# Performance work log

Hardware: AMD Instinct MI355X
Metric: run time of the kernel (lower is better)

Reference implementation:

```python
import jax, jax.numpy as jnp
import numpy as np

N, M, D = 8192, 8192, 64

def setup_inputs() -> dict:
    key = jax.random.key(0)
    kx, ky = jax.random.split(key)
    x = jax.random.normal(kx, (N, D), dtype=jnp.float32)
    y = jax.random.normal(ky, (M, D), dtype=jnp.float32)
    return {"x": x, "y": y}

def reference(x, y):
    T = 1.0
    # Dmat = 2 - euclidean cdist(x, y), computed via the Gram trick.
    sq = (jnp.sum(x * x, axis=1)[:, None]
          + jnp.sum(y * y, axis=1)[None, :]
          - 2.0 * (x @ y.T))
    Dmat = 2.0 - jnp.sqrt(jnp.maximum(sq, 0.0))          # [N, M]
    logprob_rows = jax.nn.log_softmax(Dmat * T, axis=1)   # [N, M]
    logprob_cols = jax.nn.log_softmax(Dmat.T * T, axis=1) # [M, N]
    choice_rows = jnp.argmax(logprob_rows, axis=1)        # [N]
    choice_cols = jnp.argmax(logprob_cols, axis=1)        # [M]
    seq = jnp.arange(M, dtype=choice_cols.dtype)
    mutual = choice_rows[choice_cols] == seq              # [M] bool
    lp_rows = jnp.take_along_axis(logprob_rows, choice_rows[:, None], axis=1)[:, 0]  # [N]
    lp_cols = jnp.take_along_axis(logprob_cols, choice_cols[:, None], axis=1)[:, 0]  # [M]
    # Padded (jit-friendly) form of the boolean compaction: entries where
    # mutual is False are zeroed; mutual mask identifies valid matches.
    log_probs = jnp.where(mutual, lp_rows[choice_cols] + lp_cols, 0.0)  # [M]
    dmatches = jnp.stack([choice_cols, seq], axis=1)      # [M, 2]
    return (log_probs, dmatches, mutual)
```

## Files before the change

### kernel.cpp

```cpp
#include <hip/hip_runtime.h>
#include <stdint.h>

#define NROWS 8192
#define MCOLS 8192
#define DDIM  64

typedef _Float16 half8   __attribute__((ext_vector_type(8)));
typedef float    floatx4 __attribute__((ext_vector_type(4)));

__device__ __forceinline__ unsigned f2key(float f) {
  unsigned u = __float_as_uint(f);
  return (u & 0x80000000u) ? ~u : (u | 0x80000000u);
}
__device__ __forceinline__ float key2f(unsigned k) {
  unsigned u = (k & 0x80000000u) ? (k & 0x7fffffffu) : ~k;
  return __uint_as_float(u);
}

__global__ void convert_kernel(const float* __restrict__ x, const float* __restrict__ y,
                               _Float16* __restrict__ xh, _Float16* __restrict__ xl,
                               _Float16* __restrict__ yh, _Float16* __restrict__ yl,
                               float* __restrict__ xn, float* __restrict__ yn,
                               unsigned long long* __restrict__ rk,
                               unsigned long long* __restrict__ ck,
                               float* __restrict__ rs, float* __restrict__ cs) {
  __shared__ float lnorm[32];
  const int gid = blockIdx.x * 256 + threadIdx.x;
  if (gid < 8192) { rk[gid] = 0ull; rs[gid] = 0.0f; ck[gid] = 0ull; cs[gid] = 0.0f; }
  if (threadIdx.x < 32) lnorm[threadIdx.x] = 0.0f;
  __syncthreads();

  const float* src; _Float16 *dh, *dl; float* nout; int t, rowbase;
  if (gid < 65536) { src = x; dh = xh; dl = xl; nout = xn; t = gid;
                     rowbase = blockIdx.x * 32; }
  else             { src = y; dh = yh; dl = yl; nout = yn; t = gid - 65536;
                     rowbase = (blockIdx.x - 256) * 32; }

  const int lane = t & 63;
  const int c    = (t >> 6) & 1;
  const int p    = t >> 7;
  const int row  = p * 16 + (lane & 15);
  const int k0   = c * 32 + ((lane >> 4) << 3);
  const float* s = src + (size_t)row * DDIM + k0;

  _Float16 hbuf[8], lbuf[8];
  float s8 = 0.0f;
  #pragma unroll
  for (int j = 0; j < 8; ++j) {
    float f = s[j];
    _Float16 h = (_Float16)f;
    hbuf[j] = h;
    lbuf[j] = (_Float16)((f - (float)h) * 2048.0f);
    s8 = fmaf(f, f, s8);
  }
  size_t o = (size_t)t * 8;
  *(half8*)(dh + o) = *(half8*)hbuf;
  *(half8*)(dl + o) = *(half8*)lbuf;

  atomicAdd(&lnorm[((p & 1) << 4) | (t & 15)], s8);
  __syncthreads();
  if (threadIdx.x < 32) nout[rowbase + threadIdx.x] = lnorm[threadIdx.x];
}

__global__ __launch_bounds__(256, 4) void mfma_tile_kernel(
    const _Float16* __restrict__ xh, const _Float16* __restrict__ xl,
    const _Float16* __restrict__ yh, const _Float16* __restrict__ yl,
    const float* __restrict__ xn, const float* __restrict__ yn,
    unsigned long long* __restrict__ row_key, float* __restrict__ row_sum,
    unsigned long long* __restrict__ col_key, float* __restrict__ col_sum)
{
  __shared__ unsigned long long lkey[256];
  __shared__ float              lsum[256];

  const int wave = threadIdx.x >> 6;
  const int lane = threadIdx.x & 63;
  const int l15  = lane & 15;
  const int g    = lane >> 4;
  const int ap0  = blockIdx.y * 8 + wave * 2;
  const int ro   = ap0 * 16 + g * 4;
  const int colbase = blockIdx.x * 256;

  lkey[threadIdx.x] = 0ull;
  lsum[threadIdx.x] = 0.0f;
  __syncthreads();

  const half8* xh8 = (const half8*)xh;
  const half8* xl8 = (const half8*)xl;
  const half8* yh8 = (const half8*)yh;
  const half8* yl8 = (const half8*)yl;
  const size_t a0 = (size_t)ap0 * 128 + lane;
  half8 Ah[2][2], Al[2][2];
  #pragma unroll
  for (int p = 0; p < 2; ++p) {
    Ah[p][0] = xh8[a0 + p * 128];      Ah[p][1] = xh8[a0 + p * 128 + 64];
    Al[p][0] = xl8[a0 + p * 128];      Al[p][1] = xl8[a0 + p * 128 + 64];
  }

  float xne[8], rsum[8], rmax[8]; int ridx[8];
  #pragma unroll
  for (int s = 0; s < 8; ++s) {
    xne[s]  = xn[ro + ((s >> 2) << 4) + (s & 3)];
    rsum[s] = 0.0f; rmax[s] = -3.4e38f; ridx[s] = 0;
  }

  for (int jt = 0; jt < 16; ++jt) {
    const size_t b0 = (size_t)(blockIdx.x * 16 + jt) * 128 + lane;
    const half8 bh0 = yh8[b0], bh1 = yh8[b0 + 64];
    const half8 bl0 = yl8[b0], bl1 = yl8[b0 + 64];
    const int col = colbase + jt * 16 + l15;
    const float ync = yn[col];

    float dv[8], ev[8];
    #pragma unroll
    for (int p = 0; p < 2; ++p) {
      floatx4 c1 = {}, c2 = {};
      c1 = __builtin_amdgcn_mfma_f32_16x16x32_f16(Ah[p][0], bh0, c1, 0, 0, 0);
      c1 = __builtin_amdgcn_mfma_f32_16x16x32_f16(Ah[p][1], bh1, c1, 0, 0, 0);
      c2 = __builtin_amdgcn_mfma_f32_16x16x32_f16(Al[p][0], bh0, c2, 0, 0, 0);
      c2 = __builtin_amdgcn_mfma_f32_16x16x32_f16(Al[p][1], bh1, c2, 0, 0, 0);
      c2 = __builtin_amdgcn_mfma_f32_16x16x32_f16(Ah[p][0], bl0, c2, 0, 0, 0);
      c2 = __builtin_amdgcn_mfma_f32_16x16x32_f16(Ah[p][1], bl1, c2, 0, 0, 0);
      #pragma unroll
      for (int r = 0; r < 4; ++r) {
        const int s = p * 4 + r;
        float dot = fmaf(c2[r], (1.0f / 2048.0f), c1[r]);
        float sq  = fmaxf(fmaf(-2.0f, dot, xne[s] + ync), 0.0f);
        float d   = 2.0f - __builtin_amdgcn_sqrtf(sq);
        float e   = __expf(d);
        rsum[s] += e;
        if (d > rmax[s]) ridx[s] = col;
        rmax[s] = fmaxf(rmax[s], d);
        dv[s] = d; ev[s] = e;
      }
    }

    float m01 = fmaxf(dv[0], dv[1]); int i01 = dv[1] > dv[0] ? 1 : 0;
    float m23 = fmaxf(dv[2], dv[3]); int i23 = dv[3] > dv[2] ? 3 : 2;
    float m45 = fmaxf(dv[4], dv[5]); int i45 = dv[5] > dv[4] ? 5 : 4;
    float m67 = fmaxf(dv[6], dv[7]); int i67 = dv[7] > dv[6] ? 7 : 6;
    float mA  = fmaxf(m01, m23);     int iA  = m23 > m01 ? i23 : i01;
    float mB  = fmaxf(m45, m67);     int iB  = m67 > m45 ? i67 : i45;
    float mC  = fmaxf(mA, mB);       int iC  = mB  > mA  ? iB  : iA;
    int crow  = ro + ((iC >> 2) << 4) + (iC & 3);
    float csum = ((ev[0] + ev[1]) + (ev[2] + ev[3])) + ((ev[4] + ev[5]) + (ev[6] + ev[7]));
    unsigned long long ckey =
        ((unsigned long long)f2key(mC) << 32) | (unsigned long long)(unsigned)(~(unsigned)crow);
    atomicMax(&lkey[jt * 16 + l15], ckey);
    atomicAdd(&lsum[jt * 16 + l15], csum);
  }

  unsigned long long rkk[8];
  #pragma unroll
  for (int s = 0; s < 8; ++s)
    rkk[s] = ((unsigned long long)f2key(rmax[s]) << 32) |
             (unsigned long long)(unsigned)(~(unsigned)ridx[s]);
  #pragma unroll
  for (int off = 1; off < 16; off <<= 1) {
    #pragma unroll
    for (int s = 0; s < 8; ++s) {
      rsum[s] += __shfl_xor(rsum[s], off);
      unsigned long long o = __shfl_xor(rkk[s], off);
      if (o > rkk[s]) rkk[s] = o;
    }
  }
  if (l15 == 0) {
    #pragma unroll
    for (int s = 0; s < 8; ++s) {
      int row = ro + ((s >> 2) << 4) + (s & 3);
      atomicMax(row_key + row, rkk[s]);
      atomicAdd(row_sum + row, rsum[s]);
    }
  }

  __syncthreads();
  {
    int col = colbase + threadIdx.x;
    atomicMax(col_key + col, lkey[threadIdx.x]);
    atomicAdd(col_sum + col, lsum[threadIdx.x]);
  }
}

__global__ void finalize_kernel(const unsigned long long* __restrict__ row_key,
                                const float* __restrict__ row_sum,
                                const unsigned long long* __restrict__ col_key,
                                const float* __restrict__ col_sum,
                                float* __restrict__ out)
{
  int j = blockIdx.x * 256 + threadIdx.x;
  if (j >= MCOLS) return;
  unsigned long long ck = col_key[j];
  int   ci   = (int)(~(unsigned)ck);
  float cmax = key2f((unsigned)(ck >> 32));
  float lp_col = cmax - logf(col_sum[j]);

  unsigned long long rk = row_key[ci];
  int   rj   = (int)(~(unsigned)rk);
  float rmax = key2f((unsigned)(rk >> 32));
  float lp_row = rmax - logf(row_sum[ci]);

  int mut = (rj == j);
  out[j]                 = mut ? (lp_row + lp_col) : 0.0f;
  out[MCOLS + 2 * j + 0] = (float)ci;
  out[MCOLS + 2 * j + 1] = (float)j;
  out[3 * MCOLS + j]     = mut ? 1.0f : 0.0f;
}

extern "C" void kernel_launch(void* const* d_in, const int* in_sizes, int n_in,
                              void* d_out, int out_size, void* d_ws, size_t ws_size,
                              hipStream_t stream) {
  const float* x = (const float*)d_in[0];
  const float* y = (const float*)d_in[1];
  float* out = (float*)d_out;

  char* ws = (char*)d_ws;
  unsigned long long* row_key = (unsigned long long*)(ws);
  unsigned long long* col_key = (unsigned long long*)(ws + 65536);
  float* row_sum = (float*)(ws + 131072);
  float* col_sum = (float*)(ws + 163840);
  float* xn      = (float*)(ws + 196608);
  float* yn      = (float*)(ws + 229376);
  _Float16* xh = (_Float16*)(ws + 262144);
  _Float16* xl = (_Float16*)(ws + 262144 + 1048576);
  _Float16* yh = (_Float16*)(ws + 262144 + 2097152);
  _Float16* yl = (_Float16*)(ws + 262144 + 3145728);

  convert_kernel<<<512, 256, 0, stream>>>(x, y, xh, xl, yh, yl, xn, yn,
                                          row_key, col_key, row_sum, col_sum);
  dim3 grid(MCOLS / 256, NROWS / 128);
  mfma_tile_kernel<<<grid, 256, 0, stream>>>(xh, xl, yh, yl, xn, yn,
                                             row_key, row_sum, col_key, col_sum);
  finalize_kernel<<<32, 256, 0, stream>>>(row_key, row_sum, col_key, col_sum, out);
}
```

Baseline: 128.3 us.

## Fuse finalize into tile kernel via last-block counter, widen column tile, prefetch B

Doubles the columns each block covers, which halves the grid and the global column atomics per element. It also prefetches the next B fragment in registers and folds the column max and sum into the inner loop in place of a tree reduction. The separate finalize kernel is removed: a global done counter elects the last block to compute outputs. The risk is that this last block runs the 8192-element epilogue alone, serialised at the end, and the halved grid (1024 blocks) may reduce occupancy and latency hiding.

```diff
diff --git a/kernel.cpp b/kernel.cpp
--- a/kernel.cpp
+++ b/kernel.cpp
@@ -23,10 +23,12 @@
                                float* __restrict__ xn, float* __restrict__ yn,
                                unsigned long long* __restrict__ rk,
                                unsigned long long* __restrict__ ck,
-                               float* __restrict__ rs, float* __restrict__ cs) {
+                               float* __restrict__ rs, float* __restrict__ cs,
+                               unsigned* __restrict__ done) {
   __shared__ float lnorm[32];
   const int gid = blockIdx.x * 256 + threadIdx.x;
   if (gid < 8192) { rk[gid] = 0ull; rs[gid] = 0.0f; ck[gid] = 0ull; cs[gid] = 0.0f; }
+  if (gid == 0) *done = 0u;
   if (threadIdx.x < 32) lnorm[threadIdx.x] = 0.0f;
   __syncthreads();
 
@@ -67,10 +69,12 @@
     const _Float16* __restrict__ yh, const _Float16* __restrict__ yl,
     const float* __restrict__ xn, const float* __restrict__ yn,
     unsigned long long* __restrict__ row_key, float* __restrict__ row_sum,
-    unsigned long long* __restrict__ col_key, float* __restrict__ col_sum)
+    unsigned long long* __restrict__ col_key, float* __restrict__ col_sum,
+    unsigned* __restrict__ done, float* __restrict__ out)
 {
-  __shared__ unsigned long long lkey[256];
-  __shared__ float              lsum[256];
+  __shared__ unsigned long long lkey[512];
+  __shared__ float              lsum[512];
+  __shared__ unsigned           lastflag;
 
   const int wave = threadIdx.x >> 6;
   const int lane = threadIdx.x & 63;
@@ -78,10 +82,12 @@
   const int g    = lane >> 4;
   const int ap0  = blockIdx.y * 8 + wave * 2;
   const int ro   = ap0 * 16 + g * 4;
-  const int colbase = blockIdx.x * 256;
-
-  lkey[threadIdx.x] = 0ull;
-  lsum[threadIdx.x] = 0.0f;
+  const int colbase = blockIdx.x * 512;
+
+  lkey[threadIdx.x]       = 0ull;
+  lkey[threadIdx.x + 256] = 0ull;
+  lsum[threadIdx.x]       = 0.0f;
+  lsum[threadIdx.x + 256] = 0.0f;
   __syncthreads();
 
   const half8* xh8 = (const half8*)xh;
@@ -103,14 +109,21 @@
     rsum[s] = 0.0f; rmax[s] = -3.4e38f; ridx[s] = 0;
   }
 
-  for (int jt = 0; jt < 16; ++jt) {
-    const size_t b0 = (size_t)(blockIdx.x * 16 + jt) * 128 + lane;
-    const half8 bh0 = yh8[b0], bh1 = yh8[b0 + 64];
-    const half8 bl0 = yl8[b0], bl1 = yl8[b0 + 64];
+  const size_t bbase = (size_t)(blockIdx.x * 32) * 128 + lane;
+  half8 nbh0 = yh8[bbase], nbh1 = yh8[bbase + 64];
+  half8 nbl0 = yl8[bbase], nbl1 = yl8[bbase + 64];
+
+  for (int jt = 0; jt < 32; ++jt) {
+    const half8 bh0 = nbh0, bh1 = nbh1, bl0 = nbl0, bl1 = nbl1;
     const int col = colbase + jt * 16 + l15;
     const float ync = yn[col];
-
-    float dv[8], ev[8];
+    if (jt < 31) {
+      const size_t nb = bbase + (size_t)(jt + 1) * 128;
+      nbh0 = yh8[nb];  nbh1 = yh8[nb + 64];
+      nbl0 = yl8[nb];  nbl1 = yl8[nb + 64];
+    }
+
+    float csum = 0.0f, cmax = -3.4e38f; int cs8 = 0;
     #pragma unroll
     for (int p = 0; p < 2; ++p) {
       floatx4 c1 = {}, c2 = {};
@@ -127,24 +140,17 @@
         float sq  = fmaxf(fmaf(-2.0f, dot, xne[s] + ync), 0.0f);
         float d   = 2.0f - __builtin_amdgcn_sqrtf(sq);
         float e   = __expf(d);
-        rsum[s] += e;
+        rsum[s] += e;  csum += e;
         if (d > rmax[s]) ridx[s] = col;
         rmax[s] = fmaxf(rmax[s], d);
-        dv[s] = d; ev[s] = e;
+        if (d > cmax) cs8 = s;
+        cmax = fmaxf(cmax, d);
       }
     }
 
-    float m01 = fmaxf(dv[0], dv[1]); int i01 = dv[1] > dv[0] ? 1 : 0;
-    float m23 = fmaxf(dv[2], dv[3]); int i23 = dv[3] > dv[2] ? 3 : 2;
-    float m45 = fmaxf(dv[4], dv[5]); int i45 = dv[5] > dv[4] ? 5 : 4;
-    float m67 = fmaxf(dv[6], dv[7]); int i67 = dv[7] > dv[6] ? 7 : 6;
-    float mA  = fmaxf(m01, m23);     int iA  = m23 > m01 ? i23 : i01;
-    float mB  = fmaxf(m45, m67);     int iB  = m67 > m45 ? i67 : i45;
-    float mC  = fmaxf(mA, mB);       int iC  = mB  > mA  ? iB  : iA;
-    int crow  = ro + ((iC >> 2) << 4) + (iC & 3);
-    float csum = ((ev[0] + ev[1]) + (ev[2] + ev[3])) + ((ev[4] + ev[5]) + (ev[6] + ev[7]));
+    int crow = ro + ((cs8 >> 2) << 4) + (cs8 & 3);
     unsigned long long ckey =
-        ((unsigned long long)f2key(mC) << 32) | (unsigned long long)(unsigned)(~(unsigned)crow);
+        ((unsigned long long)f2key(cmax) << 32) | (unsigned long long)(unsigned)(~(unsigned)crow);
     atomicMax(&lkey[jt * 16 + l15], ckey);
     atomicAdd(&lsum[jt * 16 + l15], csum);
   }
@@ -173,36 +179,43 @@
   }
 
   __syncthreads();
-  {
-    int col = colbase + threadIdx.x;
-    atomicMax(col_key + col, lkey[threadIdx.x]);
-    atomicAdd(col_sum + col, lsum[threadIdx.x]);
-  }
-}
-
-__global__ void finalize_kernel(const unsigned long long* __restrict__ row_key,
-                                const float* __restrict__ row_sum,
-                                const unsigned long long* __restrict__ col_key,
-                                const float* __restrict__ col_sum,
-                                float* __restrict__ out)
-{
-  int j = blockIdx.x * 256 + threadIdx.x;
-  if (j >= MCOLS) return;
-  unsigned long long ck = col_key[j];
-  int   ci   = (int)(~(unsigned)ck);
-  float cmax = key2f((unsigned)(ck >> 32));
-  float lp_col = cmax - logf(col_sum[j]);
-
-  unsigned long long rk = row_key[ci];
-  int   rj   = (int)(~(unsigned)rk);
-  float rmax = key2f((unsigned)(rk >> 32));
-  float lp_row = rmax - logf(row_sum[ci]);
-
-  int mut = (rj == j);
-  out[j]                 = mut ? (lp_row + lp_col) : 0.0f;
-  out[MCOLS + 2 * j + 0] = (float)ci;
-  out[MCOLS + 2 * j + 1] = (float)j;
-  out[3 * MCOLS + j]     = mut ? 1.0f : 0.0f;
+  #pragma unroll
+  for (int q = 0; q < 2; ++q) {
+    int t = threadIdx.x + q * 256;
+    atomicMax(col_key + colbase + t, lkey[t]);
+    atomicAdd(col_sum + colbase + t, lsum[t]);
+  }
+
+  __threadfence();
+  if (threadIdx.x == 0)
+    lastflag = (atomicAdd(done, 1u) == (16u * 64u - 1u)) ? 1u : 0u;
+  __syncthreads();
+  if (lastflag) {
+    __threadfence();
+    for (int j = threadIdx.x; j < MCOLS; j += 256) {
+      unsigned long long ck =
+          __hip_atomic_load(col_key + j, __ATOMIC_RELAXED, __HIP_MEMORY_SCOPE_AGENT);
+      float csv =
+          __hip_atomic_load(col_sum + j, __ATOMIC_RELAXED, __HIP_MEMORY_SCOPE_AGENT);
+      int   ci   = (int)(~(unsigned)ck);
+      float cmax = key2f((unsigned)(ck >> 32));
+      float lp_col = cmax - logf(csv);
+
+      unsigned long long rk =
+          __hip_atomic_load(row_key + ci, __ATOMIC_RELAXED, __HIP_MEMORY_SCOPE_AGENT);
+      float rsv =
+          __hip_atomic_load(row_sum + ci, __ATOMIC_RELAXED, __HIP_MEMORY_SCOPE_AGENT);
+      int   rj   = (int)(~(unsigned)rk);
+      float rmx  = key2f((unsigned)(rk >> 32));
+      float lp_row = rmx - logf(rsv);
+
+      int mut = (rj == j);
+      out[j]                 = mut ? (lp_row + lp_col) : 0.0f;
+      out[MCOLS + 2 * j + 0] = (float)ci;
+      out[MCOLS + 2 * j + 1] = (float)j;
+      out[3 * MCOLS + j]     = mut ? 1.0f : 0.0f;
+    }
+  }
 }
 
 extern "C" void kernel_launch(void* const* d_in, const int* in_sizes, int n_in,
@@ -223,11 +236,12 @@
   _Float16* xl = (_Float16*)(ws + 262144 + 1048576);
   _Float16* yh = (_Float16*)(ws + 262144 + 2097152);
   _Float16* yl = (_Float16*)(ws + 262144 + 3145728);
+  unsigned* done = (unsigned*)(ws + 262144 + 4194304);
 
   convert_kernel<<<512, 256, 0, stream>>>(x, y, xh, xl, yh, yl, xn, yn,
-                                          row_key, col_key, row_sum, col_sum);
-  dim3 grid(MCOLS / 256, NROWS / 128);
+                                          row_key, col_key, row_sum, col_sum, done);
+  dim3 grid(MCOLS / 512, NROWS / 128);
   mfma_tile_kernel<<<grid, 256, 0, stream>>>(xh, xl, yh, yl, xn, yn,
-                                             row_key, row_sum, col_key, col_sum);
-  finalize_kernel<<<32, 256, 0, stream>>>(row_key, row_sum, col_key, col_sum, out);
-}
+                                             row_key, row_sum, col_key, col_sum,
+                                             done, out);
+}
```

Measured after the change: 189.2 us. 47.5% more time.

## Prefetch next B tile in MFMA loop, simplify convert kernel and column argmax

Applied to the files above, without the earlier changes.

The MFMA tile loop now loads the next column tile's fp16 hi/lo fragments one iteration ahead, so global load latency overlaps with the current tile's compute. The per-tile column max/argmax and sum are tracked incrementally instead of through a stored array and a tree reduction. The convert kernel is rewritten to one element per thread with a wave shuffle reduction for the row norms, replacing LDS atomics, and is launched with more blocks. Risks: prefetching raises register pressure under launch bounds of 4 blocks per CU, and the scalar 2-byte stores in convert are less coalesced than the previous 16-byte vector stores.

```diff
diff --git a/kernel.cpp b/kernel.cpp
--- a/kernel.cpp
+++ b/kernel.cpp
@@ -24,42 +24,26 @@
                                unsigned long long* __restrict__ rk,
                                unsigned long long* __restrict__ ck,
                                float* __restrict__ rs, float* __restrict__ cs) {
-  __shared__ float lnorm[32];
-  const int gid = blockIdx.x * 256 + threadIdx.x;
-  if (gid < 8192) { rk[gid] = 0ull; rs[gid] = 0.0f; ck[gid] = 0ull; cs[gid] = 0.0f; }
-  if (threadIdx.x < 32) lnorm[threadIdx.x] = 0.0f;
-  __syncthreads();
-
-  const float* src; _Float16 *dh, *dl; float* nout; int t, rowbase;
-  if (gid < 65536) { src = x; dh = xh; dl = xl; nout = xn; t = gid;
-                     rowbase = blockIdx.x * 32; }
-  else             { src = y; dh = yh; dl = yl; nout = yn; t = gid - 65536;
-                     rowbase = (blockIdx.x - 256) * 32; }
-
-  const int lane = t & 63;
-  const int c    = (t >> 6) & 1;
-  const int p    = t >> 7;
-  const int row  = p * 16 + (lane & 15);
-  const int k0   = c * 32 + ((lane >> 4) << 3);
-  const float* s = src + (size_t)row * DDIM + k0;
-
-  _Float16 hbuf[8], lbuf[8];
-  float s8 = 0.0f;
-  #pragma unroll
-  for (int j = 0; j < 8; ++j) {
-    float f = s[j];
-    _Float16 h = (_Float16)f;
-    hbuf[j] = h;
-    lbuf[j] = (_Float16)((f - (float)h) * 2048.0f);
-    s8 = fmaf(f, f, s8);
-  }
-  size_t o = (size_t)t * 8;
-  *(half8*)(dh + o) = *(half8*)hbuf;
-  *(half8*)(dl + o) = *(half8*)lbuf;
-
-  atomicAdd(&lnorm[((p & 1) << 4) | (t & 15)], s8);
-  __syncthreads();
-  if (threadIdx.x < 32) nout[rowbase + threadIdx.x] = lnorm[threadIdx.x];
+  const int gid  = blockIdx.x * 256 + threadIdx.x;
+  if (gid < NROWS) { rk[gid] = 0ull; rs[gid] = 0.0f; ck[gid] = 0ull; cs[gid] = 0.0f; }
+
+  const int row  = gid >> 6;
+  const int k    = threadIdx.x & 63;
+  const float* src; _Float16 *dh, *dl; float* nout; int r;
+  if (row < NROWS) { src = x; dh = xh; dl = xl; nout = xn; r = row; }
+  else             { src = y; dh = yh; dl = yl; nout = yn; r = row - NROWS; }
+
+  float f = src[(size_t)r * DDIM + k];
+  _Float16 h = (_Float16)f;
+  _Float16 l = (_Float16)((f - (float)h) * 2048.0f);
+  int pos = ((r >> 4) << 10) + ((k >> 5) << 9) + ((((k >> 3) & 3) << 4) + (r & 15)) * 8 + (k & 7);
+  dh[pos] = h;
+  dl[pos] = l;
+
+  float s = f * f;
+  #pragma unroll
+  for (int off = 32; off > 0; off >>= 1) s += __shfl_down(s, off);
+  if (k == 0) nout[r] = s;
 }
 
 __global__ __launch_bounds__(256, 4) void mfma_tile_kernel(
@@ -103,14 +87,21 @@
     rsum[s] = 0.0f; rmax[s] = -3.4e38f; ridx[s] = 0;
   }
 
+  const size_t bbase = (size_t)(blockIdx.x * 16) * 128 + lane;
+  half8 nbh0 = yh8[bbase], nbh1 = yh8[bbase + 64];
+  half8 nbl0 = yl8[bbase], nbl1 = yl8[bbase + 64];
+
   for (int jt = 0; jt < 16; ++jt) {
-    const size_t b0 = (size_t)(blockIdx.x * 16 + jt) * 128 + lane;
-    const half8 bh0 = yh8[b0], bh1 = yh8[b0 + 64];
-    const half8 bl0 = yl8[b0], bl1 = yl8[b0 + 64];
+    const half8 bh0 = nbh0, bh1 = nbh1, bl0 = nbl0, bl1 = nbl1;
     const int col = colbase + jt * 16 + l15;
     const float ync = yn[col];
-
-    float dv[8], ev[8];
+    if (jt < 15) {
+      const size_t nb = bbase + (size_t)(jt + 1) * 128;
+      nbh0 = yh8[nb];  nbh1 = yh8[nb + 64];
+      nbl0 = yl8[nb];  nbl1 = yl8[nb + 64];
+    }
+
+    float csum = 0.0f, cmax = -3.4e38f; int cs8 = 0;
     #pragma unroll
     for (int p = 0; p < 2; ++p) {
       floatx4 c1 = {}, c2 = {};
@@ -127,24 +118,17 @@
         float sq  = fmaxf(fmaf(-2.0f, dot, xne[s] + ync), 0.0f);
         float d   = 2.0f - __builtin_amdgcn_sqrtf(sq);
         float e   = __expf(d);
-        rsum[s] += e;
+        rsum[s] += e;  csum += e;
         if (d > rmax[s]) ridx[s] = col;
         rmax[s] = fmaxf(rmax[s], d);
-        dv[s] = d; ev[s] = e;
+        if (d > cmax) cs8 = s;
+        cmax = fmaxf(cmax, d);
       }
     }
 
-    float m01 = fmaxf(dv[0], dv[1]); int i01 = dv[1] > dv[0] ? 1 : 0;
-    float m23 = fmaxf(dv[2], dv[3]); int i23 = dv[3] > dv[2] ? 3 : 2;
-    float m45 = fmaxf(dv[4], dv[5]); int i45 = dv[5] > dv[4] ? 5 : 4;
-    float m67 = fmaxf(dv[6], dv[7]); int i67 = dv[7] > dv[6] ? 7 : 6;
-    float mA  = fmaxf(m01, m23);     int iA  = m23 > m01 ? i23 : i01;
-    float mB  = fmaxf(m45, m67);     int iB  = m67 > m45 ? i67 : i45;
-    float mC  = fmaxf(mA, mB);       int iC  = mB  > mA  ? iB  : iA;
-    int crow  = ro + ((iC >> 2) << 4) + (iC & 3);
-    float csum = ((ev[0] + ev[1]) + (ev[2] + ev[3])) + ((ev[4] + ev[5]) + (ev[6] + ev[7]));
+    int crow = ro + ((cs8 >> 2) << 4) + (cs8 & 3);
     unsigned long long ckey =
-        ((unsigned long long)f2key(mC) << 32) | (unsigned long long)(unsigned)(~(unsigned)crow);
+        ((unsigned long long)f2key(cmax) << 32) | (unsigned long long)(unsigned)(~(unsigned)crow);
     atomicMax(&lkey[jt * 16 + l15], ckey);
     atomicAdd(&lsum[jt * 16 + l15], csum);
   }
@@ -224,8 +208,8 @@
   _Float16* yh = (_Float16*)(ws + 262144 + 2097152);
   _Float16* yl = (_Float16*)(ws + 262144 + 3145728);
 
-  convert_kernel<<<512, 256, 0, stream>>>(x, y, xh, xl, yh, yl, xn, yn,
-                                          row_key, col_key, row_sum, col_sum);
+  convert_kernel<<<4096, 256, 0, stream>>>(x, y, xh, xl, yh, yl, xn, yn,
+                                           row_key, col_key, row_sum, col_sum);
   dim3 grid(MCOLS / 256, NROWS / 128);
   mfma_tile_kernel<<<grid, 256, 0, stream>>>(xh, xl, yh, yl, xn, yn,
                                              row_key, row_sum, col_key, col_sum);
```

Result: no change. 129.4 us (+0.8%).
